# Kernel optimization log

Hardware: AMD Instinct MI355X
Metric: run time of the kernel (lower is better)

The kernel has to match this reference:

```python
import jax, jax.numpy as jnp
import numpy as np

N_EL = 16
N_NUC = 4
N_FEATS = 32
CUTOFF = 10.0
ION_POT = 0.5
ALPHA = 1.0
BATCH = 32768
HIDDEN = 64
I_IDX, J_IDX = np.triu_indices(N_EL, 1)  # electron pairs i<j
N_PAIRS = N_EL * N_NUC + N_EL * (N_EL - 1) // 2
D_IN = N_PAIRS * N_FEATS


def ssp(x):
    # shifted softplus: softplus(x) - log(2), so ssp(0) = 0
    return jax.nn.softplus(x) - jnp.log(2.0).astype(x.dtype)


def setup_inputs() -> dict:
    key = jax.random.key(0)
    ks = jax.random.split(key, 9)
    rs = jax.random.normal(ks[0], (BATCH, N_EL, 3), jnp.float32) * 2.0
    coords = jax.random.normal(ks[1], (N_NUC, 3), jnp.float32)
    charges = jnp.arange(1, N_NUC + 1, dtype=jnp.float32)
    W1 = jax.random.normal(ks[2], (D_IN, HIDDEN), jnp.float32) / jnp.sqrt(D_IN)
    b1 = jnp.zeros((HIDDEN,), jnp.float32)
    W2 = jax.random.normal(ks[3], (HIDDEN, HIDDEN), jnp.float32) / jnp.sqrt(HIDDEN)
    b2 = jnp.zeros((HIDDEN,), jnp.float32)
    W3 = jax.random.normal(ks[4], (HIDDEN, 1), jnp.float32) / jnp.sqrt(HIDDEN)
    b3 = jnp.zeros((1,), jnp.float32)
    return {"rs": rs, "coords": coords, "charges": charges,
            "W1": W1, "b1": b1, "W2": W2, "b2": b2, "W3": W3, "b3": b3}


def reference(rs, coords, charges, W1, b1, W2, b2, W3, b3):
    B = rs.shape[0]
    # electron-nucleus distances: [B, n_el, n_nuc]
    diff_nuc = rs[:, :, None, :] - coords[None, None, :, :]
    dists_nuc = jnp.sqrt(jnp.sum(diff_nuc * diff_nuc, axis=-1))
    # electron-electron distances for pairs i<j: [B, n_el*(n_el-1)//2]
    diff_el = rs[:, I_IDX, :] - rs[:, J_IDX, :]
    dists_el = jnp.sqrt(jnp.sum(diff_el * diff_el, axis=-1))
    dists = jnp.concatenate([dists_nuc.reshape(B, -1), dists_el], axis=1)  # [B, N_PAIRS]
    # Gaussian distance basis expansion
    qs = jnp.linspace(0.0, 1.0, N_FEATS, dtype=rs.dtype)
    mus = CUTOFF * qs ** 2
    sigmas = (1.0 + CUTOFF * qs) / 7.0
    xs = jnp.exp(-((dists[..., None] - mus) ** 2) / sigmas ** 2)  # [B, N_PAIRS, N_FEATS]
    xs = xs.reshape(B, -1)
    # small MLP with shifted-softplus activations
    h = ssp(xs @ W1 + b1)
    h = ssp(h @ W2 + b2)
    ys = (h @ W3 + b3)[:, 0]
    # nuclear asymptotic factor
    decay = jnp.sqrt(2.0 * ION_POT)
    terms = (charges[None, None, :] * dists_nuc + decay * ALPHA * dists_nuc ** 2) / (1.0 + ALPHA * dists_nuc)
    asymp = jnp.exp(-jnp.sum(terms, axis=(1, 2)))
    return jnp.exp(ys) * asymp
```

## Files before the change

kernel.cpp:

```cpp
#include <hip/hip_runtime.h>
#include <math.h>

#define N_EL    16
#define N_NUC   4
#define N_FEATS 32
#define N_PAIRS 184
#define HIDDEN  64
#define TB      32
#define BLOCK   256
#define DLD     185
#define H1LD    68
#define TPW     23
#define WS_PART_OFF (1 << 19)

typedef int   intx8    __attribute__((ext_vector_type(8)));
typedef float floatx16 __attribute__((ext_vector_type(16)));

__constant__ unsigned char c_I[120] = {
    0,0,0,0,0,0,0,0,0,0,0,0,0,0,0,
    1,1,1,1,1,1,1,1,1,1,1,1,1,1,
    2,2,2,2,2,2,2,2,2,2,2,2,2,
    3,3,3,3,3,3,3,3,3,3,3,3,
    4,4,4,4,4,4,4,4,4,4,4,
    5,5,5,5,5,5,5,5,5,5,
    6,6,6,6,6,6,6,6,6,
    7,7,7,7,7,7,7,7,
    8,8,8,8,8,8,8,
    9,9,9,9,9,9,
    10,10,10,10,10,
    11,11,11,11,
    12,12,12,
    13,13,
    14
};
__constant__ unsigned char c_J[120] = {
    1,2,3,4,5,6,7,8,9,10,11,12,13,14,15,
    2,3,4,5,6,7,8,9,10,11,12,13,14,15,
    3,4,5,6,7,8,9,10,11,12,13,14,15,
    4,5,6,7,8,9,10,11,12,13,14,15,
    5,6,7,8,9,10,11,12,13,14,15,
    6,7,8,9,10,11,12,13,14,15,
    7,8,9,10,11,12,13,14,15,
    8,9,10,11,12,13,14,15,
    9,10,11,12,13,14,15,
    10,11,12,13,14,15,
    11,12,13,14,15,
    12,13,14,15,
    13,14,15,
    14,15,
    15
};

__device__ __forceinline__ float ssp(float x) {
    float a = fabsf(x);
    return fmaxf(x, 0.0f) + log1pf(__expf(-a)) - 0.69314718056f;
}
__device__ __forceinline__ float redg(float v) {
    v += __shfl_xor(v, 1);
    v += __shfl_xor(v, 2);
    v += __shfl_xor(v, 4);
    return v;
}

__global__ __launch_bounds__(256)
void prep_w1_kernel(const float* __restrict__ W1, intx8* __restrict__ ws)
{
    __shared__ float w[2 * N_FEATS * HIDDEN];
    const int t = blockIdx.x;
    const float* src = W1 + (size_t)(2 * t) * (N_FEATS * HIDDEN);
    for (int k = threadIdx.x; k < 2 * N_FEATS * HIDDEN; k += 256) w[k] = src[k];
    __syncthreads();

    const int tid = threadIdx.x;
    if (tid >= 128) return;
    const int lane = tid & 63;
    const int nh   = tid >> 6;
    const int lh   = lane >> 5;
    const int col  = nh * 32 + (lane & 31);
    const int fb   = lh * 16;
    intx8 frag;
#pragma unroll
    for (int r = 0; r < 8; ++r) {
        const int pair = r >> 2;
        const int fo   = fb + ((r & 3) << 2);
        const float v0 = 64.0f * w[(pair * N_FEATS + fo + 0) * 64 + col];
        const float v1 = 64.0f * w[(pair * N_FEATS + fo + 1) * 64 + col];
        const float v2 = 64.0f * w[(pair * N_FEATS + fo + 2) * 64 + col];
        const float v3 = 64.0f * w[(pair * N_FEATS + fo + 3) * 64 + col];
        int d = __builtin_amdgcn_cvt_pk_fp8_f32(v0, v1, 0, false);
        d     = __builtin_amdgcn_cvt_pk_fp8_f32(v2, v3, d, true);
        frag[r] = d;
    }
    ws[(size_t)(t * 2 + nh) * 64 + lane] = frag;
}

__global__ __launch_bounds__(BLOCK)
void wfnet_gemm(const float* __restrict__ rs,
                const float* __restrict__ coords,
                const intx8* __restrict__ ws,
                float* __restrict__ partials)
{
    __shared__ float lds_rs[TB * N_EL * 3];
    __shared__ float lds_dist[TB * DLD];

    const int tid  = threadIdx.x;
    const int wave = tid >> 6;
    const int lane = tid & 63;
    const int m    = lane & 31;
    const int lh   = lane >> 5;

    {
        const float* rs_blk = rs + (size_t)blockIdx.x * (TB * N_EL * 3);
        for (int k = tid; k < TB * N_EL * 3; k += BLOCK) lds_rs[k] = rs_blk[k];
    }
    __syncthreads();

    {
        const int bl = tid >> 3, g = tid & 7;
        const float* myrs = lds_rs + bl * (N_EL * 3);
        float* dst = lds_dist + bl * DLD;
        for (int i = 0; i < 8; ++i) {
            const int p = g + 8 * i;
            const int e = p >> 2, n = p & 3;
            const float dx = myrs[e * 3 + 0] - coords[n * 3 + 0];
            const float dy = myrs[e * 3 + 1] - coords[n * 3 + 1];
            const float dz = myrs[e * 3 + 2] - coords[n * 3 + 2];
            dst[p] = sqrtf(dx * dx + dy * dy + dz * dz);
        }
        for (int i = 0; i < 15; ++i) {
            const int q  = g + 8 * i;
            const int ei = 3 * (int)c_I[q], ej = 3 * (int)c_J[q];
            const float dx = myrs[ei + 0] - myrs[ej + 0];
            const float dy = myrs[ei + 1] - myrs[ej + 1];
            const float dz = myrs[ei + 2] - myrs[ej + 2];
            dst[64 + q] = sqrtf(dx * dx + dy * dy + dz * dz);
        }
    }
    __syncthreads();

    const int f0 = lh * 16;
#define MKC(P, FF) float P##1, P##0; { \
    const float fq = (float)(FF) * (1.0f / 31.0f); \
    const float mu = 10.0f * fq * fq; \
    const float is = 7.0f / (1.0f + 10.0f * fq); \
    P##1 = is * 3.3972871404442143f; \
    P##0 = -mu * P##1; }
    MKC(F0_,  f0 + 0)  MKC(F1_,  f0 + 1)  MKC(F2_,  f0 + 2)  MKC(F3_,  f0 + 3)
    MKC(F4_,  f0 + 4)  MKC(F5_,  f0 + 5)  MKC(F6_,  f0 + 6)  MKC(F7_,  f0 + 7)
    MKC(F8_,  f0 + 8)  MKC(F9_,  f0 + 9)  MKC(F10_, f0 + 10) MKC(F11_, f0 + 11)
    MKC(F12_, f0 + 12) MKC(F13_, f0 + 13) MKC(F14_, f0 + 14) MKC(F15_, f0 + 15)
#undef MKC

    floatx16 accA = {};
    floatx16 accB = {};
    const intx8* wq = ws + ((size_t)(wave * TPW) * 128 + lane);
    const float* drow = lds_dist + m * DLD + wave * (2 * TPW);

#define XB(dd, P) ({ \
    const float t_ = fmaf(dd, P##1, P##0); \
    const float z_ = fmaf(t_, -t_, 56.5f); \
    unsigned u_; \
    asm("v_cvt_u32_f32 %0, %1" : "=v"(u_) : "v"(z_)); \
    u_; })
#define PK4(dd, A, B, C, D) \
    (int)(XB(dd, A) | (XB(dd, B) << 8) | (XB(dd, C) << 16) | (XB(dd, D) << 24))
#define MKA8(AV, dx0, dx1) \
    intx8 AV; { \
    AV[0] = PK4(dx0, F0_,  F1_,  F2_,  F3_);  \
    AV[1] = PK4(dx0, F4_,  F5_,  F6_,  F7_);  \
    AV[2] = PK4(dx0, F8_,  F9_,  F10_, F11_); \
    AV[3] = PK4(dx0, F12_, F13_, F14_, F15_); \
    AV[4] = PK4(dx1, F0_,  F1_,  F2_,  F3_);  \
    AV[5] = PK4(dx1, F4_,  F5_,  F6_,  F7_);  \
    AV[6] = PK4(dx1, F8_,  F9_,  F10_, F11_); \
    AV[7] = PK4(dx1, F12_, F13_, F14_, F15_); }
#define KROUND(AV, Q0, Q1) { \
    accA = __builtin_amdgcn_mfma_scale_f32_32x32x64_f8f6f4( \
               AV, Q0, accA, 0, 0, 0, 0x7F7F7F7F, 0, 0x79797979); \
    accB = __builtin_amdgcn_mfma_scale_f32_32x32x64_f8f6f4( \
               AV, Q1, accB, 0, 0, 0, 0x7F7F7F7F, 0, 0x79797979); }

    intx8 pA0 = wq[0],   pA1 = wq[64];
    intx8 pB0 = wq[128], pB1 = wq[192];
    float dA0 = drow[0], dA1 = drow[1];
    float dB0 = drow[2], dB1 = drow[3];

    for (int it = 0; it < 10; ++it) {
        const intx8* wn = wq + 256;
        const float eA0 = drow[4 * it + 4], eA1 = drow[4 * it + 5];
        const float eB0 = drow[4 * it + 6], eB1 = drow[4 * it + 7];

        { MKA8(av, dA0, dA1) KROUND(av, pA0, pA1) }
        pA0 = wn[0]; pA1 = wn[64];

        { MKA8(bv, dB0, dB1) KROUND(bv, pB0, pB1) }
        pB0 = wn[128]; pB1 = wn[192];

        wq = wn;
        dA0 = eA0; dA1 = eA1; dB0 = eB0; dB1 = eB1;
    }
    {
        const intx8* wn = wq + 256;
        const float eA0 = drow[44], eA1 = drow[45];
        { MKA8(av, dA0, dA1) KROUND(av, pA0, pA1) }
        pA0 = wn[0]; pA1 = wn[64];
        { MKA8(bv, dB0, dB1) KROUND(bv, pB0, pB1) }
        { MKA8(cv, eA0, eA1) KROUND(cv, pA0, pA1) }
    }
#undef KROUND
#undef MKA8
#undef PK4
#undef XB

    float* pdst = partials + ((size_t)blockIdx.x * 4 + wave) * 2048;
#pragma unroll
    for (int rg = 0; rg < 16; ++rg) {
        const int el = (rg & 3) + 8 * (rg >> 2) + 4 * lh;
        pdst[el * 64 + m]      = accA[rg];
        pdst[el * 64 + 32 + m] = accB[rg];
    }
}

__global__ __launch_bounds__(BLOCK)
void wfnet_tail(const float* __restrict__ rs,
                const float* __restrict__ coords,
                const float* __restrict__ charges,
                const float* __restrict__ partials,
                const float* __restrict__ b1,
                const float* __restrict__ W2,
                const float* __restrict__ b2,
                const float* __restrict__ W3,
                const float* __restrict__ b3,
                float* __restrict__ out)
{
    __shared__ float lds_rs[TB * N_EL * 3];
    __shared__ float lds_h1[TB * H1LD];

    const int tid = threadIdx.x;
    const int el  = tid >> 3;
    const int g   = tid & 7;
    const int b   = blockIdx.x * TB + el;

    {
        const float* rs_blk = rs + (size_t)blockIdx.x * (TB * N_EL * 3);
        for (int k = tid; k < TB * N_EL * 3; k += BLOCK) lds_rs[k] = rs_blk[k];
    }

    {
        const float* pb = partials + (size_t)blockIdx.x * 8192 + el * 64 + g * 8;
        const float4 p00 = ((const float4*)(pb + 0 * 2048))[0];
        const float4 p01 = ((const float4*)(pb + 0 * 2048))[1];
        const float4 p10 = ((const float4*)(pb + 1 * 2048))[0];
        const float4 p11 = ((const float4*)(pb + 1 * 2048))[1];
        const float4 p20 = ((const float4*)(pb + 2 * 2048))[0];
        const float4 p21 = ((const float4*)(pb + 2 * 2048))[1];
        const float4 p30 = ((const float4*)(pb + 3 * 2048))[0];
        const float4 p31 = ((const float4*)(pb + 3 * 2048))[1];
        const float4 ba = ((const float4*)(b1 + g * 8))[0];
        const float4 bb = ((const float4*)(b1 + g * 8))[1];
        float* h1w = lds_h1 + el * H1LD + g * 8;
        h1w[0] = ssp(p00.x + p10.x + p20.x + p30.x + ba.x);
        h1w[1] = ssp(p00.y + p10.y + p20.y + p30.y + ba.y);
        h1w[2] = ssp(p00.z + p10.z + p20.z + p30.z + ba.z);
        h1w[3] = ssp(p00.w + p10.w + p20.w + p30.w + ba.w);
        h1w[4] = ssp(p01.x + p11.x + p21.x + p31.x + bb.x);
        h1w[5] = ssp(p01.y + p11.y + p21.y + p31.y + bb.y);
        h1w[6] = ssp(p01.z + p11.z + p21.z + p31.z + bb.z);
        h1w[7] = ssp(p01.w + p11.w + p21.w + p31.w + bb.w);
    }

    float asy = 0.0f;
    __syncthreads();
    {
        const float* myrs = lds_rs + el * (N_EL * 3);
        const float4 ch = *(const float4*)charges;
#pragma unroll
        for (int i = 0; i < 8; ++i) {
            const int p = g + 8 * i;
            const int e = p >> 2, n = p & 3;
            const float dx = myrs[e * 3 + 0] - coords[n * 3 + 0];
            const float dy = myrs[e * 3 + 1] - coords[n * 3 + 1];
            const float dz = myrs[e * 3 + 2] - coords[n * 3 + 2];
            const float d = sqrtf(dx * dx + dy * dy + dz * dz);
            const float Z = (n < 2) ? ((n == 0) ? ch.x : ch.y)
                                    : ((n == 2) ? ch.z : ch.w);
            asy += (Z * d + d * d) / (1.0f + d);
        }
    }
    asy = redg(asy);

    const float4* __restrict__ W2v = (const float4*)W2;
    const float4* __restrict__ b2v = (const float4*)b2;
    const int wbi = g * 2;
    const float4 b2a = b2v[wbi], b2b = b2v[wbi + 1];
    float s0 = b2a.x, s1 = b2a.y, s2 = b2a.z, s3 = b2a.w;
    float s4 = b2b.x, s5 = b2b.y, s6 = b2b.z, s7 = b2b.w;

    const float* __restrict__ h1row = lds_h1 + el * H1LD;
    for (int k = 0; k < HIDDEN; ++k) {
        const float hk  = h1row[k];
        const float4 wa = W2v[k * 16 + wbi];
        const float4 wb = W2v[k * 16 + wbi + 1];
        s0 = fmaf(hk, wa.x, s0); s1 = fmaf(hk, wa.y, s1);
        s2 = fmaf(hk, wa.z, s2); s3 = fmaf(hk, wa.w, s3);
        s4 = fmaf(hk, wb.x, s4); s5 = fmaf(hk, wb.y, s5);
        s6 = fmaf(hk, wb.z, s6); s7 = fmaf(hk, wb.w, s7);
    }

    const float4* __restrict__ W3v = (const float4*)W3;
    const float4 w3a = W3v[wbi], w3b = W3v[wbi + 1];
    float part = ssp(s0) * w3a.x + ssp(s1) * w3a.y
               + ssp(s2) * w3a.z + ssp(s3) * w3a.w
               + ssp(s4) * w3b.x + ssp(s5) * w3b.y
               + ssp(s6) * w3b.z + ssp(s7) * w3b.w;
    part = redg(part);

    if (g == 0) {
        const float ys = part + b3[0];
        out[b] = __expf(ys) * __expf(-asy);
    }
}

extern "C" void kernel_launch(void* const* d_in, const int* in_sizes, int n_in,
                              void* d_out, int out_size, void* d_ws, size_t ws_size,
                              hipStream_t stream) {
    const float* rs      = (const float*)d_in[0];
    const float* coords  = (const float*)d_in[1];
    const float* charges = (const float*)d_in[2];
    const float* W1      = (const float*)d_in[3];
    const float* b1      = (const float*)d_in[4];
    const float* W2      = (const float*)d_in[5];
    const float* b2      = (const float*)d_in[6];
    const float* W3      = (const float*)d_in[7];
    const float* b3      = (const float*)d_in[8];
    float* out = (float*)d_out;

    const int batch = in_sizes[0] / (N_EL * 3);
    intx8* w1f8     = (intx8*)d_ws;
    float* partials = (float*)((char*)d_ws + WS_PART_OFF);

    prep_w1_kernel<<<N_PAIRS / 2, 256, 0, stream>>>(W1, w1f8);
    wfnet_gemm<<<batch / TB, BLOCK, 0, stream>>>(rs, coords, w1f8, partials);
    wfnet_tail<<<batch / TB, BLOCK, 0, stream>>>(rs, coords, charges, partials,
                                                 b1, W2, b2, W3, b3, out);
}
```

Baseline: 139.1 us.

## Pack FP8 features with cvt_pk_u8 and stage W2 in shared memory

In the main layer-1 kernel, the per-feature convert-and-shift-or byte packing is replaced with the v_cvt_pk_u8_f32 builtin, which converts each value and inserts it into its byte lane in one instruction. This removes the shift and OR work from the VALU-heavy feature expansion. Separately, the tail kernel copies W2 (16 KB) into LDS and runs the layer-2 loop from there instead of from global memory. That adds LDS use per block and relies on a barrier that must already exist before the loop. The clamping and rounding of cvt_pk_u8 may differ slightly from v_cvt_u32_f32.

```diff
diff --git a/kernel.cpp b/kernel.cpp
--- a/kernel.cpp
+++ b/kernel.cpp
@@ -156,24 +156,24 @@
     const intx8* wq = ws + ((size_t)(wave * TPW) * 128 + lane);
     const float* drow = lds_dist + m * DLD + wave * (2 * TPW);
 
-#define XB(dd, P) ({ \
-    const float t_ = fmaf(dd, P##1, P##0); \
-    const float z_ = fmaf(t_, -t_, 56.5f); \
-    unsigned u_; \
-    asm("v_cvt_u32_f32 %0, %1" : "=v"(u_) : "v"(z_)); \
-    u_; })
-#define PK4(dd, A, B, C, D) \
-    (int)(XB(dd, A) | (XB(dd, B) << 8) | (XB(dd, C) << 16) | (XB(dd, D) << 24))
+#define XZ(dd, P) ({ const float t_ = fmaf(dd, P##1, P##0); fmaf(t_, -t_, 56.5f); })
+#define PKD(dd, A, B, C, D) ({ \
+    unsigned w_; \
+    w_ = __builtin_amdgcn_cvt_pk_u8_f32(XZ(dd, A), 0, 0u); \
+    w_ = __builtin_amdgcn_cvt_pk_u8_f32(XZ(dd, B), 1, w_); \
+    w_ = __builtin_amdgcn_cvt_pk_u8_f32(XZ(dd, C), 2, w_); \
+    w_ = __builtin_amdgcn_cvt_pk_u8_f32(XZ(dd, D), 3, w_); \
+    (int)w_; })
 #define MKA8(AV, dx0, dx1) \
     intx8 AV; { \
-    AV[0] = PK4(dx0, F0_,  F1_,  F2_,  F3_);  \
-    AV[1] = PK4(dx0, F4_,  F5_,  F6_,  F7_);  \
-    AV[2] = PK4(dx0, F8_,  F9_,  F10_, F11_); \
-    AV[3] = PK4(dx0, F12_, F13_, F14_, F15_); \
-    AV[4] = PK4(dx1, F0_,  F1_,  F2_,  F3_);  \
-    AV[5] = PK4(dx1, F4_,  F5_,  F6_,  F7_);  \
-    AV[6] = PK4(dx1, F8_,  F9_,  F10_, F11_); \
-    AV[7] = PK4(dx1, F12_, F13_, F14_, F15_); }
+    AV[0] = PKD(dx0, F0_,  F1_,  F2_,  F3_);  \
+    AV[1] = PKD(dx0, F4_,  F5_,  F6_,  F7_);  \
+    AV[2] = PKD(dx0, F8_,  F9_,  F10_, F11_); \
+    AV[3] = PKD(dx0, F12_, F13_, F14_, F15_); \
+    AV[4] = PKD(dx1, F0_,  F1_,  F2_,  F3_);  \
+    AV[5] = PKD(dx1, F4_,  F5_,  F6_,  F7_);  \
+    AV[6] = PKD(dx1, F8_,  F9_,  F10_, F11_); \
+    AV[7] = PKD(dx1, F12_, F13_, F14_, F15_); }
 #define KROUND(AV, Q0, Q1) { \
     accA = __builtin_amdgcn_mfma_scale_f32_32x32x64_f8f6f4( \
                AV, Q0, accA, 0, 0, 0, 0x7F7F7F7F, 0, 0x79797979); \
@@ -209,8 +209,8 @@
     }
 #undef KROUND
 #undef MKA8
-#undef PK4
-#undef XB
+#undef PKD
+#undef XZ
 
     float* pdst = partials + ((size_t)blockIdx.x * 4 + wave) * 2048;
 #pragma unroll
@@ -235,6 +235,7 @@
 {
     __shared__ float lds_rs[TB * N_EL * 3];
     __shared__ float lds_h1[TB * H1LD];
+    __shared__ float lds_w2[HIDDEN * HIDDEN];
 
     const int tid = threadIdx.x;
     const int el  = tid >> 3;
@@ -244,6 +245,12 @@
     {
         const float* rs_blk = rs + (size_t)blockIdx.x * (TB * N_EL * 3);
         for (int k = tid; k < TB * N_EL * 3; k += BLOCK) lds_rs[k] = rs_blk[k];
+    }
+    {
+        float4* dst = (float4*)lds_w2;
+        const float4* src = (const float4*)W2;
+#pragma unroll
+        for (int i = 0; i < 4; ++i) dst[tid + 256 * i] = src[tid + 256 * i];
     }
 
     {
@@ -289,7 +296,7 @@
     }
     asy = redg(asy);
 
-    const float4* __restrict__ W2v = (const float4*)W2;
+    const float4* __restrict__ W2v = (const float4*)lds_w2;
     const float4* __restrict__ b2v = (const float4*)b2;
     const int wbi = g * 2;
     const float4 b2a = b2v[wbi], b2b = b2v[wbi + 1];
```

Result: faster. 128.7 us, median of 2 (-7.5%).
